# Performance work log

Measured on AMD Instinct MI355X. Metric: run time of the kernel, lower is better.

The kernel has to match this reference:

```python
import math
import jax, jax.numpy as jnp
import numpy as np

N_STEPS = 4
D_ENERGY = 128
FEATURE_DIM = 1024
B, N = 4, 2048


def setup_inputs() -> dict:
    key = jax.random.key(0)
    ks = jax.random.split(key, 5)
    scale = 1.0 / math.sqrt(FEATURE_DIM)
    return {
        "features": jax.random.normal(ks[0], (B, N, FEATURE_DIM), dtype=jnp.float32),
        "W_q": jax.random.normal(ks[1], (FEATURE_DIM, D_ENERGY), dtype=jnp.float32) * scale,
        "W_k": jax.random.normal(ks[2], (FEATURE_DIM, D_ENERGY), dtype=jnp.float32) * scale,
        "charge_w": jax.random.normal(ks[3], (FEATURE_DIM, 1), dtype=jnp.float32) * scale,
        "charge_b": jnp.zeros((1,), dtype=jnp.float32),
        "locality_scale": jnp.float32(1.0),
        "step_size": jnp.float32(0.5),
        "charge_decay": jnp.float32(0.3),
    }


def reference(features, W_q, W_k, charge_w, charge_b, locality_scale, step_size, charge_decay):
    Bn, Nn, _ = features.shape
    # compatibility: [B,N,N]
    Q = jnp.einsum("bnf,fe->bne", features, W_q)
    K = jnp.einsum("bnf,fe->bne", features, W_k)
    compat = jnp.einsum("bqe,bke->bqk", Q, K) / jnp.sqrt(jnp.float32(D_ENERGY))
    # locality bias: locality_scale / max(|i-j|, 1)
    pos = jnp.arange(Nn, dtype=jnp.float32)
    dist = jnp.maximum(jnp.abs(pos[None, :] - pos[:, None]), 1.0)
    locality = locality_scale / dist  # [N,N]
    # initial charge in (0,1): [B,N]
    charge = jax.nn.sigmoid(jnp.einsum("bnf,fo->bno", features, charge_w)[..., 0] + charge_b[0])
    base = compat + locality[None]  # [B,N,N], fixed across steps
    logits = base
    for _ in range(N_STEPS):
        attn = jax.nn.softmax(logits, axis=-1)
        received = attn.sum(axis=-2)  # [B,N] column sums
        charge = charge * (1.0 - charge_decay * jax.nn.sigmoid(received - 1.0))
        energy = -base * charge[..., :, None] * charge[..., None, :]
        logits = logits - step_size * energy
    return jax.nn.softmax(logits, axis=-1)
```

## Files before the change

### kernel.cpp

```cpp
#include <hip/hip_runtime.h>
#include <math.h>

namespace {
constexpr int NB = 4;
constexpr int NN = 2048;
constexpr int FD = 1024;
constexpr int DE = 128;
constexpr int BN = NB * NN;

constexpr size_t WSW_OFF   = 0;
constexpr size_t FH_OFF    = 8388608;
constexpr size_t FL_OFF    = 12582912;
constexpr size_t QKHL_OFF  = 16777216;
constexpr size_t C_OFF     = QKHL_OFF + 2097152;
}

typedef __attribute__((ext_vector_type(8))) short bf16x8;
typedef __attribute__((ext_vector_type(4))) float f32x4;
typedef __attribute__((ext_vector_type(8))) _Float16 f16x8;

__device__ __forceinline__ unsigned short bf16_hi(float x) {
    unsigned u = __float_as_uint(x);
    unsigned r = (u + 0x7fffu + ((u >> 16) & 1u)) >> 16;
    return (unsigned short)r;
}
__device__ __forceinline__ float bf16_val(unsigned short h) {
    return __uint_as_float((unsigned)h << 16);
}


__global__ __launch_bounds__(256) void prep(
        const float* __restrict__ feat, const float* __restrict__ Wq,
        const float* __restrict__ Wk, const float* __restrict__ cw,
        const float* __restrict__ cbias,
        unsigned short* __restrict__ Fh, unsigned short* __restrict__ Fl,
        unsigned short* __restrict__ Wqh, unsigned short* __restrict__ Wql,
        unsigned short* __restrict__ Wkh, unsigned short* __restrict__ Wkl,
        float* __restrict__ c0) {
    const int bid = blockIdx.x;
    const int tid = threadIdx.x;
    if (bid < 4096) {
        const int g = bid * 256 + tid;
        const int tile = g >> 6, lane = g & 63;
        const int tr = tile >> 5, fc = tile & 31;
        const int row = tr * 16 + (lane & 15);
        const int f0 = fc * 32 + (lane >> 4) * 8;
        const float* src = &feat[(size_t)row * FD + f0];
        ushort4 h0, l0, h1, l1;
        float4 a = *(const float4*)src;
        float4 b = *(const float4*)(src + 4);
        h0.x = bf16_hi(a.x); l0.x = bf16_hi(a.x - bf16_val(h0.x));
        h0.y = bf16_hi(a.y); l0.y = bf16_hi(a.y - bf16_val(h0.y));
        h0.z = bf16_hi(a.z); l0.z = bf16_hi(a.z - bf16_val(h0.z));
        h0.w = bf16_hi(a.w); l0.w = bf16_hi(a.w - bf16_val(h0.w));
        h1.x = bf16_hi(b.x); l1.x = bf16_hi(b.x - bf16_val(h1.x));
        h1.y = bf16_hi(b.y); l1.y = bf16_hi(b.y - bf16_val(h1.y));
        h1.z = bf16_hi(b.z); l1.z = bf16_hi(b.z - bf16_val(h1.z));
        h1.w = bf16_hi(b.w); l1.w = bf16_hi(b.w - bf16_val(h1.w));
        const size_t dst = (size_t)tile * 512 + lane * 8;
        *(ushort4*)&Fh[dst] = h0; *(ushort4*)&Fh[dst + 4] = h1;
        *(ushort4*)&Fl[dst] = l0; *(ushort4*)&Fl[dst + 4] = l1;
    } else if (bid < 4224) {
        const int wbid = bid - 4096;
        const int mat = wbid >> 6;
        const int g = (wbid & 63) * 256 + tid;
        const int tile = g >> 6, lane = g & 63;
        const int ec = tile >> 5, fc = tile & 31;
        const int e = ec * 16 + (lane & 15);
        const int f0 = fc * 32 + (lane >> 4) * 8;
        const float* W = mat ? Wk : Wq;
        unsigned short* Th = mat ? Wkh : Wqh;
        unsigned short* Tl = mat ? Wkl : Wql;
        unsigned short hh[8], ll[8];
        #pragma unroll
        for (int j = 0; j < 8; ++j) {
            float v = W[(size_t)(f0 + j) * DE + e];
            hh[j] = bf16_hi(v); ll[j] = bf16_hi(v - bf16_val(hh[j]));
        }
        const size_t dst = (size_t)tile * 512 + lane * 8;
        *(ushort4*)&Th[dst]     = make_ushort4(hh[0], hh[1], hh[2], hh[3]);
        *(ushort4*)&Th[dst + 4] = make_ushort4(hh[4], hh[5], hh[6], hh[7]);
        *(ushort4*)&Tl[dst]     = make_ushort4(ll[0], ll[1], ll[2], ll[3]);
        *(ushort4*)&Tl[dst + 4] = make_ushort4(ll[4], ll[5], ll[6], ll[7]);
    } else {
        const int wave = tid >> 6, lane = tid & 63;
        const int r = (bid - 4224) * 4 + wave;
        const float* fr = feat + (size_t)r * FD;
        float s = 0.f;
        #pragma unroll
        for (int k = 0; k < 16; ++k) { int f = lane + 64 * k; s += fr[f] * cw[f]; }
        for (int off = 32; off > 0; off >>= 1) s += __shfl_xor(s, off);
        if (lane == 0) {
            float x = s + cbias[0];
            c0[r] = 1.f / (1.f + __expf(-x));
        }
    }
}

__global__ __launch_bounds__(256) void qk_proj(
        const unsigned short* __restrict__ Fh, const unsigned short* __restrict__ Fl,
        const unsigned short* __restrict__ Wqh, const unsigned short* __restrict__ Wql,
        const unsigned short* __restrict__ Wkh, const unsigned short* __restrict__ Wkl,
        unsigned short* __restrict__ Qh, unsigned short* __restrict__ Ql,
        unsigned short* __restrict__ Kh, unsigned short* __restrict__ Kl) {
    __shared__ unsigned short lds[8192];
    const int tid = threadIdx.x;
    const int w = tid >> 6, lane = tid & 63;
    const int quad = lane >> 4, l16 = lane & 15;
    const int blk = blockIdx.x;
    const int mat = w >> 1, ec0 = (w & 1) * 4;
    const unsigned short* Bh = mat ? Wkh : Wqh;
    const unsigned short* Bl = mat ? Wkl : Wql;

    f32x4 acc[4];
    #pragma unroll
    for (int c = 0; c < 4; ++c) acc[c] = (f32x4){0.f, 0.f, 0.f, 0.f};

    for (int fc = 0; fc < 32; ++fc) {
        const size_t aoff = ((size_t)(blk * 32 + fc) * 64 + lane) * 8;
        bf16x8 aH = *(const bf16x8*)&Fh[aoff];
        bf16x8 aL = *(const bf16x8*)&Fl[aoff];
        #pragma unroll
        for (int ct = 0; ct < 4; ++ct) {
            const size_t boff = ((size_t)((ec0 + ct) * 32 + fc) * 64 + lane) * 8;
            bf16x8 bH = *(const bf16x8*)&Bh[boff];
            bf16x8 bL = *(const bf16x8*)&Bl[boff];
            acc[ct] = __builtin_amdgcn_mfma_f32_16x16x32_bf16(aH, bH, acc[ct], 0, 0, 0);
            acc[ct] = __builtin_amdgcn_mfma_f32_16x16x32_bf16(aH, bL, acc[ct], 0, 0, 0);
            acc[ct] = __builtin_amdgcn_mfma_f32_16x16x32_bf16(aL, bH, acc[ct], 0, 0, 0);
        }
    }
    #pragma unroll
    for (int ct = 0; ct < 4; ++ct) {
        const int e = (ec0 + ct) * 16 + l16;
        const int kc = e >> 5, q2 = (e >> 3) & 3, j2 = e & 7;
        #pragma unroll
        for (int reg = 0; reg < 4; ++reg) {
            const int rl = quad * 4 + reg;
            const float v = acc[ct][reg];
            const unsigned short h = bf16_hi(v);
            const unsigned short l = bf16_hi(v - bf16_val(h));
            const int idx = (kc * 64 + q2 * 16 + rl) * 8 + j2;
            lds[(mat * 2 + 0) * 2048 + idx] = h;
            lds[(mat * 2 + 1) * 2048 + idx] = l;
        }
    }
    __syncthreads();
    const size_t gbase = (size_t)blk * 2048;
    unsigned short* const dsts[4] = {Qh, Ql, Kh, Kl};
    #pragma unroll
    for (int ch = 0; ch < 4; ++ch) {
        const int o = ch * 2048 + tid * 8;
        unsigned short* dst = dsts[ch] + gbase + tid * 8;
        *(ushort4*)&dst[0] = *(const ushort4*)&lds[o];
        *(ushort4*)&dst[4] = *(const ushort4*)&lds[o + 4];
    }
}

__global__ __launch_bounds__(256) void base_mfma(
        const unsigned short* __restrict__ Qh, const unsigned short* __restrict__ Ql,
        const unsigned short* __restrict__ Kh, const unsigned short* __restrict__ Kl,
        const float* __restrict__ d_ls, _Float16* __restrict__ baseH) {
    const int tid = threadIdx.x;
    const int w = tid >> 6, lane = tid & 63;
    const int quad = lane >> 4, l16 = lane & 15;
    const int b = blockIdx.z;
    const int i0 = blockIdx.y * 128, j0 = blockIdx.x * 128;
    const int trA0 = (b * NN + i0) / 16 + w * 2;
    const int trB0 = (b * NN + j0) / 16;

    f32x4 acc[2][8];
    #pragma unroll
    for (int a = 0; a < 2; ++a)
        #pragma unroll
        for (int c = 0; c < 8; ++c) acc[a][c] = (f32x4){0.f, 0.f, 0.f, 0.f};

    #pragma unroll
    for (int kc = 0; kc < 4; ++kc) {
        bf16x8 aH[2], aL[2];
        #pragma unroll
        for (int rt = 0; rt < 2; ++rt) {
            const size_t off = ((size_t)((trA0 + rt) * 4 + kc) * 64 + lane) * 8;
            aH[rt] = *(const bf16x8*)&Qh[off];
            aL[rt] = *(const bf16x8*)&Ql[off];
        }
        #pragma unroll
        for (int ct = 0; ct < 8; ++ct) {
            const size_t off = ((size_t)((trB0 + ct) * 4 + kc) * 64 + lane) * 8;
            bf16x8 bH = *(const bf16x8*)&Kh[off];
            bf16x8 bL = *(const bf16x8*)&Kl[off];
            #pragma unroll
            for (int rt = 0; rt < 2; ++rt) {
                acc[rt][ct] = __builtin_amdgcn_mfma_f32_16x16x32_bf16(aH[rt], bH, acc[rt][ct], 0, 0, 0);
                acc[rt][ct] = __builtin_amdgcn_mfma_f32_16x16x32_bf16(aH[rt], bL, acc[rt][ct], 0, 0, 0);
                acc[rt][ct] = __builtin_amdgcn_mfma_f32_16x16x32_bf16(aL[rt], bH, acc[rt][ct], 0, 0, 0);
            }
        }
    }
    const float ls = d_ls[0];
    const float rs = 0.08838834764831845f;
    #pragma unroll
    for (int rt = 0; rt < 2; ++rt)
        #pragma unroll
        for (int reg = 0; reg < 4; ++reg) {
            const int i = i0 + w * 32 + rt * 16 + quad * 4 + reg;
            _Float16* brow = baseH + ((size_t)b * NN + i) * NN;
            #pragma unroll
            for (int ct = 0; ct < 8; ++ct) {
                const int j = j0 + ct * 16 + l16;
                const float dist = fmaxf(fabsf((float)(i - j)), 1.0f);
                brow[j] = (_Float16)(acc[rt][ct][reg] * rs + ls / dist);
            }
        }
}

template <int T, bool WO>
__global__ __launch_bounds__(256) void step_pass(
        const _Float16* __restrict__ base, const float* __restrict__ charge,
        const float* __restrict__ d_ss, float* __restrict__ P,
        float* __restrict__ out) {
    constexpr int TS = T > 0 ? T : 1;
    __shared__ float wsum[2][4];
    const int tid = threadIdx.x;
    const int w = tid >> 6, lane = tid & 63;
    const int blk = blockIdx.x;
    const int b = blk >> 8;
    const int r0 = (blk & 255) * 8;
    const float ss = d_ss[0];
    const size_t cb = (size_t)b << 11;
    const int c0 = tid * 8;

    float cjv[TS][8];
    #pragma unroll
    for (int u = 0; u < T; ++u) {
        const float* s = &charge[(size_t)(u + 1) * BN + cb + c0];
        const float4 a0 = *(const float4*)&s[0];
        const float4 a1 = *(const float4*)&s[4];
        cjv[u][0] = a0.x; cjv[u][1] = a0.y; cjv[u][2] = a0.z; cjv[u][3] = a0.w;
        cjv[u][4] = a1.x; cjv[u][5] = a1.y; cjv[u][6] = a1.z; cjv[u][7] = a1.w;
    }

    float col_acc[8];
    if (!WO) {
        #pragma unroll
        for (int j = 0; j < 8; ++j) col_acc[j] = 0.f;
    }

    const _Float16* bp = base + (cb + r0) * NN + c0;
    f16x8 hv = *(const f16x8*)bp;

    #pragma unroll
    for (int r = 0; r < 8; ++r) {
        f16x8 hvn;
        if (r < 7) hvn = *(const f16x8*)(bp + (size_t)(r + 1) * NN);
        const size_t ri = cb + r0 + r;
        float ci[TS];
        #pragma unroll
        for (int u = 0; u < T; ++u)
            ci[u] = charge[(size_t)(u + 1) * BN + ri] * ss;

        float x[8];
        float ps = 0.f;
        #pragma unroll
        for (int j = 0; j < 8; ++j) {
            float m = 1.f;
            #pragma unroll
            for (int u = 0; u < T; ++u) m += ci[u] * cjv[u][j];
            const float v = __expf((float)hv[j] * m);
            x[j] = v;
            ps += v;
        }
        #pragma unroll
        for (int off = 32; off > 0; off >>= 1) ps += __shfl_xor(ps, off);
        if (lane == 0) wsum[r & 1][w] = ps;
        __syncthreads();
        const float inv = 1.f / (wsum[r & 1][0] + wsum[r & 1][1] +
                                 wsum[r & 1][2] + wsum[r & 1][3]);

        if (WO) {
            float4 o0 = {x[0] * inv, x[1] * inv, x[2] * inv, x[3] * inv};
            float4 o1 = {x[4] * inv, x[5] * inv, x[6] * inv, x[7] * inv};
            float* op = &out[ri * NN + c0];
            *(float4*)&op[0] = o0;
            *(float4*)&op[4] = o1;
        } else {
            #pragma unroll
            for (int j = 0; j < 8; ++j) col_acc[j] += x[j] * inv;
        }
        hv = hvn;
    }

    if (!WO) {
        float* prow = P + (size_t)blk * NN + c0;
        *(float4*)&prow[0] = *(float4*)&col_acc[0];
        *(float4*)&prow[4] = *(float4*)&col_acc[4];
    }
}

__global__ __launch_bounds__(256) void charge_reduce(
        const float* __restrict__ P, const float* __restrict__ d_decay,
        const float* __restrict__ c_prev, float* __restrict__ c_next) {
    const int b = blockIdx.x >> 3;
    const int col = ((blockIdx.x & 7) << 8) + threadIdx.x;
    const float* p = P + ((size_t)b * 256) * NN + col;
    float s = 0.f;
    #pragma unroll 8
    for (int r = 0; r < 256; ++r) s += p[(size_t)r * NN];
    const int gi = (b << 11) + col;
    const float sg = 1.f / (1.f + __expf(1.f - s));
    c_next[gi] = c_prev[gi] * (1.f - d_decay[0] * sg);
}

extern "C" void kernel_launch(void* const* d_in, const int* in_sizes, int n_in,
                              void* d_out, int out_size, void* d_ws, size_t ws_size,
                              hipStream_t stream) {
    const float* feat  = (const float*)d_in[0];
    const float* Wq    = (const float*)d_in[1];
    const float* Wk    = (const float*)d_in[2];
    const float* cw    = (const float*)d_in[3];
    const float* cb    = (const float*)d_in[4];
    const float* ls    = (const float*)d_in[5];
    const float* ssp   = (const float*)d_in[6];
    const float* decay = (const float*)d_in[7];

    float* ws   = (float*)d_ws;
    unsigned short* Fh = (unsigned short*)(ws + FH_OFF);
    unsigned short* Fl = (unsigned short*)(ws + FL_OFF);
    unsigned short* qkhl = (unsigned short*)(ws + QKHL_OFF);
    unsigned short* Qh = qkhl;
    unsigned short* Ql = qkhl + (size_t)BN * DE;
    unsigned short* Kh = qkhl + (size_t)2 * BN * DE;
    unsigned short* Kl = qkhl + (size_t)3 * BN * DE;
    unsigned short* Wqh = (unsigned short*)(ws + WSW_OFF);
    unsigned short* Wql = Wqh + (size_t)DE * FD;
    unsigned short* Wkh = Wqh + (size_t)2 * DE * FD;
    unsigned short* Wkl = Wqh + (size_t)3 * DE * FD;
    float* charge = ws + C_OFF;
    _Float16* baseH = (_Float16*)(ws + WSW_OFF);
    float* P      = ws + FH_OFF;
    float* out    = (float*)d_out;

    prep<<<6272, 256, 0, stream>>>(feat, Wq, Wk, cw, cb,
                                   Fh, Fl, Wqh, Wql, Wkh, Wkl, charge);
    qk_proj<<<512, 256, 0, stream>>>(Fh, Fl, Wqh, Wql, Wkh, Wkl,
                                     Qh, Ql, Kh, Kl);
    base_mfma<<<dim3(NN / 128, NN / 128, NB), 256, 0, stream>>>(
        Qh, Ql, Kh, Kl, ls, baseH);

    step_pass<0, false><<<1024, 256, 0, stream>>>(baseH, charge, ssp, P, nullptr);
    charge_reduce<<<32, 256, 0, stream>>>(P, decay, charge, charge + (size_t)BN);
    step_pass<1, false><<<1024, 256, 0, stream>>>(baseH, charge, ssp, P, nullptr);
    charge_reduce<<<32, 256, 0, stream>>>(P, decay, charge + (size_t)BN, charge + (size_t)2 * BN);
    step_pass<2, false><<<1024, 256, 0, stream>>>(baseH, charge, ssp, P, nullptr);
    charge_reduce<<<32, 256, 0, stream>>>(P, decay, charge + (size_t)2 * BN, charge + (size_t)3 * BN);
    step_pass<3, false><<<1024, 256, 0, stream>>>(baseH, charge, ssp, P, nullptr);
    charge_reduce<<<32, 256, 0, stream>>>(P, decay, charge + (size_t)3 * BN, charge + (size_t)4 * BN);
    step_pass<4, true><<<1024, 256, 0, stream>>>(baseH, charge, ssp, nullptr, out);
}
```

Before: 282.0 us.

## Split qk_proj reduction dimension across four waves with LDS reduction

```diff
diff --git a/kernel.cpp b/kernel.cpp
--- a/kernel.cpp
+++ b/kernel.cpp
@@ -97,18 +97,18 @@
     }
 }
 
-__global__ __launch_bounds__(256) void qk_proj(
+__global__ __launch_bounds__(1024) void qk_proj(
         const unsigned short* __restrict__ Fh, const unsigned short* __restrict__ Fl,
         const unsigned short* __restrict__ Wqh, const unsigned short* __restrict__ Wql,
         const unsigned short* __restrict__ Wkh, const unsigned short* __restrict__ Wkl,
         unsigned short* __restrict__ Qh, unsigned short* __restrict__ Ql,
         unsigned short* __restrict__ Kh, unsigned short* __restrict__ Kl) {
-    __shared__ unsigned short lds[8192];
+    __shared__ f32x4 stage[4096];
     const int tid = threadIdx.x;
     const int w = tid >> 6, lane = tid & 63;
     const int quad = lane >> 4, l16 = lane & 15;
     const int blk = blockIdx.x;
-    const int mat = w >> 1, ec0 = (w & 1) * 4;
+    const int mat = w >> 3, ech = (w >> 2) & 1, kch = w & 3;
     const unsigned short* Bh = mat ? Wkh : Wqh;
     const unsigned short* Bl = mat ? Wkl : Wql;
 
@@ -116,13 +116,16 @@
     #pragma unroll
     for (int c = 0; c < 4; ++c) acc[c] = (f32x4){0.f, 0.f, 0.f, 0.f};
 
-    for (int fc = 0; fc < 32; ++fc) {
+    const int fc0 = kch * 8;
+    #pragma unroll 2
+    for (int f = 0; f < 8; ++f) {
+        const int fc = fc0 + f;
         const size_t aoff = ((size_t)(blk * 32 + fc) * 64 + lane) * 8;
         bf16x8 aH = *(const bf16x8*)&Fh[aoff];
         bf16x8 aL = *(const bf16x8*)&Fl[aoff];
         #pragma unroll
         for (int ct = 0; ct < 4; ++ct) {
-            const size_t boff = ((size_t)((ec0 + ct) * 32 + fc) * 64 + lane) * 8;
+            const size_t boff = ((size_t)((ech * 4 + ct) * 32 + fc) * 64 + lane) * 8;
             bf16x8 bH = *(const bf16x8*)&Bh[boff];
             bf16x8 bL = *(const bf16x8*)&Bl[boff];
             acc[ct] = __builtin_amdgcn_mfma_f32_16x16x32_bf16(aH, bH, acc[ct], 0, 0, 0);
@@ -131,30 +134,52 @@
         }
     }
     #pragma unroll
-    for (int ct = 0; ct < 4; ++ct) {
-        const int e = (ec0 + ct) * 16 + l16;
-        const int kc = e >> 5, q2 = (e >> 3) & 3, j2 = e & 7;
-        #pragma unroll
-        for (int reg = 0; reg < 4; ++reg) {
-            const int rl = quad * 4 + reg;
-            const float v = acc[ct][reg];
-            const unsigned short h = bf16_hi(v);
-            const unsigned short l = bf16_hi(v - bf16_val(h));
-            const int idx = (kc * 64 + q2 * 16 + rl) * 8 + j2;
-            lds[(mat * 2 + 0) * 2048 + idx] = h;
-            lds[(mat * 2 + 1) * 2048 + idx] = l;
-        }
-    }
+    for (int ct = 0; ct < 4; ++ct)
+        stage[(w * 4 + ct) * 64 + lane] = acc[ct];
     __syncthreads();
+
+    f32x4 red[4];
+    const bool reducer = (kch == 0);
+    if (reducer) {
+        #pragma unroll
+        for (int ct = 0; ct < 4; ++ct) {
+            f32x4 s = stage[(w * 4 + ct) * 64 + lane];
+            #pragma unroll
+            for (int k = 1; k < 4; ++k) {
+                const f32x4 t = stage[((w + k) * 4 + ct) * 64 + lane];
+                s.x += t.x; s.y += t.y; s.z += t.z; s.w += t.w;
+            }
+            red[ct] = s;
+        }
+    }
+    __syncthreads();
+
+    unsigned short* lds16 = (unsigned short*)stage;
+    if (reducer) {
+        #pragma unroll
+        for (int ct = 0; ct < 4; ++ct) {
+            const int e = (ech * 4 + ct) * 16 + l16;
+            const int kce = e >> 5, q2 = (e >> 3) & 3, j2 = e & 7;
+            #pragma unroll
+            for (int reg = 0; reg < 4; ++reg) {
+                const int rl = quad * 4 + reg;
+                const float v = red[ct][reg];
+                const unsigned short h = bf16_hi(v);
+                const unsigned short l = bf16_hi(v - bf16_val(h));
+                const int idx = (kce * 64 + q2 * 16 + rl) * 8 + j2;
+                lds16[(mat * 2 + 0) * 2048 + idx] = h;
+                lds16[(mat * 2 + 1) * 2048 + idx] = l;
+            }
+        }
+    }
+    __syncthreads();
+
+    const int ch = tid >> 8, o = (tid & 255) * 8;
     const size_t gbase = (size_t)blk * 2048;
     unsigned short* const dsts[4] = {Qh, Ql, Kh, Kl};
-    #pragma unroll
-    for (int ch = 0; ch < 4; ++ch) {
-        const int o = ch * 2048 + tid * 8;
-        unsigned short* dst = dsts[ch] + gbase + tid * 8;
-        *(ushort4*)&dst[0] = *(const ushort4*)&lds[o];
-        *(ushort4*)&dst[4] = *(const ushort4*)&lds[o + 4];
-    }
+    unsigned short* dst = dsts[ch] + gbase + o;
+    *(ushort4*)&dst[0] = *(const ushort4*)&lds16[ch * 2048 + o];
+    *(ushort4*)&dst[4] = *(const ushort4*)&lds16[ch * 2048 + o + 4];
 }
 
 __global__ __launch_bounds__(256) void base_mfma(
@@ -214,6 +239,7 @@
         }
 }
 
+__global__ void step_dummy() {}
 template <int T, bool WO>
 __global__ __launch_bounds__(256) void step_pass(
         const _Float16* __restrict__ base, const float* __restrict__ charge,
@@ -342,8 +368,8 @@
 
     prep<<<6272, 256, 0, stream>>>(feat, Wq, Wk, cw, cb,
                                    Fh, Fl, Wqh, Wql, Wkh, Wkl, charge);
-    qk_proj<<<512, 256, 0, stream>>>(Fh, Fl, Wqh, Wql, Wkh, Wkl,
-                                     Qh, Ql, Kh, Kl);
+    qk_proj<<<512, 1024, 0, stream>>>(Fh, Fl, Wqh, Wql, Wkh, Wkl,
+                                      Qh, Ql, Kh, Kl);
     base_mfma<<<dim3(NN / 128, NN / 128, NB), 256, 0, stream>>>(
         Qh, Ql, Kh, Kl, ls, baseH);
 
```

New measurement: 276.1 us. 2.1% less time.
